# Kernel tuning notes

Hardware: AMD Instinct MI355X
Metric: run time of the kernel (lower is better)

Reference implementation:

```python
import jax, jax.numpy as jnp
import numpy as np

B, C, H, W = 4, 32, 512, 512


def _warp_add(x, flow, residual):
    # x: [B,C,H,W], flow: [B,2,H,W], residual: [B,C,H,W]
    Bs, Cs, Hs, Ws = x.shape
    # align_corners=False pixel-center base grid in [-1,1]
    gy = (jnp.arange(Hs, dtype=x.dtype) + 0.5) * (2.0 / Hs) - 1.0  # [H]
    gx = (jnp.arange(Ws, dtype=x.dtype) + 0.5) * (2.0 / Ws) - 1.0  # [W]
    grid_x = gx[None, None, :] + flow[:, 0]  # [B,H,W]
    grid_y = gy[None, :, None] + flow[:, 1]  # [B,H,W]
    # circular wrap on x only
    grid_x = jnp.mod(grid_x + 1.0, 2.0) - 1.0
    real_x = (grid_x + 1.0) * (Ws * 0.5) - 0.5
    real_y = (grid_y + 1.0) * (Hs * 0.5) - 0.5
    x0 = jnp.floor(real_x)
    y0 = jnp.floor(real_y)
    dx = real_x - x0
    dy = real_y - y0
    ix0 = x0.astype(jnp.int32)
    iy0 = y0.astype(jnp.int32)
    ix1 = ix0 + 1
    iy1 = iy0 + 1

    def valid(ix, iy):
        return (ix >= 0) & (ix < Ws) & (iy >= 0) & (iy < Hs)

    xf = x.reshape(Bs, Cs, Hs * Ws)

    def gather(ix, iy):
        v = valid(ix, iy)  # [B,H,W]
        idx = jnp.clip(iy, 0, Hs - 1) * Ws + jnp.clip(ix, 0, Ws - 1)  # [B,H,W]
        g = jnp.take_along_axis(xf, idx.reshape(Bs, 1, Hs * Ws), axis=2)  # [B,C,H*W]
        g = g.reshape(Bs, Cs, Hs, Ws)
        return jnp.where(v[:, None, :, :], g, 0.0)

    v_tl = gather(ix0, iy0)
    v_tr = gather(ix1, iy0)
    v_bl = gather(ix0, iy1)
    v_br = gather(ix1, iy1)

    w_tl = ((1.0 - dx) * (1.0 - dy))[:, None]
    w_tr = (dx * (1.0 - dy))[:, None]
    w_bl = ((1.0 - dx) * dy)[:, None]
    w_br = (dx * dy)[:, None]

    out = w_tl * v_tl + w_tr * v_tr + w_bl * v_bl + w_br * v_br + residual
    return out


def setup_inputs() -> dict:
    key = jax.random.key(0)
    k1, k2, k3 = jax.random.split(key, 3)
    x = jax.random.normal(k1, (B, C, H, W), dtype=jnp.float32)
    flow = jax.random.normal(k2, (B, 2, H, W), dtype=jnp.float32) * 0.1
    residual = jax.random.normal(k3, (B, C, H, W), dtype=jnp.float32)
    return {"x": x, "flow": flow, "residual": residual}


def reference(x, flow, residual):
    return _warp_add(x, flow, residual)
```

## Files before the change

kernel.cpp:

```cpp
#include <hip/hip_runtime.h>

#define Bdim 4
#define Cdim 32
#define Hdim 512
#define Wdim 512
#define HWdim (Hdim * Wdim)

typedef __attribute__((ext_vector_type(4))) float    f32x4;
typedef __attribute__((ext_vector_type(2))) _Float16 f16x2;
typedef __attribute__((ext_vector_type(4))) _Float16 f16x4;
typedef __attribute__((ext_vector_type(8))) _Float16 f16x8;

__global__ __launch_bounds__(256) void transpose_nhwc_half_kernel(
    const float* __restrict__ x, _Float16* __restrict__ ws)
{
    __shared__ float lds[Cdim * 132];

    const int idx = blockIdx.x;
    const int tw  = idx & 3;
    const int h   = (idx >> 2) & (Hdim - 1);
    const int b   = idx >> 11;
    const int w0  = tw * 128;
    const int t   = threadIdx.x;

    f32x4 r[4];
    #pragma unroll
    for (int i = 0; i < 4; ++i) {
        const int f4 = i * 256 + t;
        const int c  = f4 >> 5;
        const int w4 = f4 & 31;
        r[i] = *(const f32x4*)(x + (((size_t)b * Cdim + c) * Hdim + h) * Wdim + w0 + w4 * 4);
    }
    #pragma unroll
    for (int i = 0; i < 4; ++i) {
        const int f4 = i * 256 + t;
        *(f32x4*)(lds + (f4 >> 5) * 132 + (f4 & 31) * 4) = r[i];
    }
    __syncthreads();

    const size_t base = (((size_t)b * Hdim + h) * Wdim + w0) * Cdim;
    const int w_ = t >> 1;
    const int c0 = (t & 1) * 16;
    f16x8 v0, v1;
    #pragma unroll
    for (int k = 0; k < 8; ++k) v0[k] = (_Float16)lds[(c0 + k) * 132 + w_];
    #pragma unroll
    for (int k = 0; k < 8; ++k) v1[k] = (_Float16)lds[(c0 + 8 + k) * 132 + w_];
    *(f16x8*)(ws + base + (size_t)w_ * Cdim + c0)     = v0;
    *(f16x8*)(ws + base + (size_t)w_ * Cdim + c0 + 8) = v1;
}

__global__ __launch_bounds__(256) void gather_nhwc_half_kernel(
    const _Float16* __restrict__ ws,
    const float* __restrict__ flow,
    const float* __restrict__ residual,
    float* __restrict__ out)
{
    __shared__ _Float16 s_buf[4 * 64 * 34];

    const int orig = blockIdx.x;
    const int idx  = (orig & 7) * 512 + (orig >> 3);

    const int b    = idx >> 10;
    const int h    = (idx >> 1) & (Hdim - 1);
    const int w0   = (idx & 1) << 8;
    const int t    = threadIdx.x;
    const int lane = t & 63;
    const int wv   = t >> 6;

    int   off0, off1, off2, off3;
    float wt0,  wt1,  wt2,  wt3;
    {
        const int w = w0 + t;
        const int pixg = h * Wdim + w;
        const float fx = flow[((size_t)b * 2 + 0) * HWdim + pixg];
        const float fy = flow[((size_t)b * 2 + 1) * HWdim + pixg];

        float gx = ((float)w + 0.5f) * (2.0f / (float)Wdim) - 1.0f + fx;
        float gy = ((float)h + 0.5f) * (2.0f / (float)Hdim) - 1.0f + fy;

        float tm = fmodf(gx + 1.0f, 2.0f);
        if (tm < 0.0f) tm += 2.0f;
        gx = tm - 1.0f;

        const float real_x = (gx + 1.0f) * ((float)Wdim * 0.5f) - 0.5f;
        const float real_y = (gy + 1.0f) * ((float)Hdim * 0.5f) - 0.5f;

        const float x0f = floorf(real_x);
        const float y0f = floorf(real_y);
        const float dx = real_x - x0f;
        const float dy = real_y - y0f;

        const int ix0 = (int)x0f;
        const int iy0 = (int)y0f;
        const int ix1 = ix0 + 1;
        const int iy1 = iy0 + 1;

        const bool vx0 = (ix0 >= 0) && (ix0 < Wdim);
        const bool vx1 = (ix1 >= 0) && (ix1 < Wdim);
        const bool vy0 = (iy0 >= 0) && (iy0 < Hdim);
        const bool vy1 = (iy1 >= 0) && (iy1 < Hdim);

        const int cx0 = min(max(ix0, 0), Wdim - 1);
        const int cx1 = min(max(ix1, 0), Wdim - 1);
        const int cy0 = min(max(iy0, 0), Hdim - 1);
        const int cy1 = min(max(iy1, 0), Hdim - 1);

        float w_tl = (1.0f - dx) * (1.0f - dy);
        float w_tr = dx * (1.0f - dy);
        float w_bl = (1.0f - dx) * dy;
        float w_br = dx * dy;
        if (!(vx0 && vy0)) w_tl = 0.0f;
        if (!(vx1 && vy0)) w_tr = 0.0f;
        if (!(vx0 && vy1)) w_bl = 0.0f;
        if (!(vx1 && vy1)) w_br = 0.0f;

        off0 = (cy0 * Wdim + cx0) * Cdim;
        off1 = (cy0 * Wdim + cx1) * Cdim;
        off2 = (cy1 * Wdim + cx0) * Cdim;
        off3 = (cy1 * Wdim + cx1) * Cdim;
        wt0 = w_tl; wt1 = w_tr; wt2 = w_bl; wt3 = w_br;
    }

    {
        const int ci = lane & 7;
        const int c0 = ci * 4;
        const int ps = lane >> 3;
        const _Float16* xb = ws + (size_t)b * (size_t)HWdim * Cdim + c0;
        _Float16* sb = s_buf + wv * (64 * 34);

        int   co[4]; float cw[4]; f16x4 cv[4];
        {
            const int sj = ps;
            co[0] = __shfl(off0, sj, 64); co[1] = __shfl(off1, sj, 64);
            co[2] = __shfl(off2, sj, 64); co[3] = __shfl(off3, sj, 64);
            cw[0] = __shfl(wt0, sj, 64);  cw[1] = __shfl(wt1, sj, 64);
            cw[2] = __shfl(wt2, sj, 64);  cw[3] = __shfl(wt3, sj, 64);
            #pragma unroll
            for (int k = 0; k < 4; ++k) cv[k] = *(const f16x4*)(xb + co[k]);
        }

        #pragma unroll
        for (int j = 0; j < 8; ++j) {
            int   no[4]; float nw[4]; f16x4 nv[4];
            if (j < 7) {
                const int sj = (j + 1) * 8 + ps;
                no[0] = __shfl(off0, sj, 64); no[1] = __shfl(off1, sj, 64);
                no[2] = __shfl(off2, sj, 64); no[3] = __shfl(off3, sj, 64);
                nw[0] = __shfl(wt0, sj, 64);  nw[1] = __shfl(wt1, sj, 64);
                nw[2] = __shfl(wt2, sj, 64);  nw[3] = __shfl(wt3, sj, 64);
                #pragma unroll
                for (int k = 0; k < 4; ++k) nv[k] = *(const f16x4*)(xb + no[k]);
            }

            const int lpix = j * 8 + ps;
            const float a0 = cw[0] * (float)cv[0][0] + cw[1] * (float)cv[1][0]
                           + cw[2] * (float)cv[2][0] + cw[3] * (float)cv[3][0];
            const float a1 = cw[0] * (float)cv[0][1] + cw[1] * (float)cv[1][1]
                           + cw[2] * (float)cv[2][1] + cw[3] * (float)cv[3][1];
            const float a2 = cw[0] * (float)cv[0][2] + cw[1] * (float)cv[1][2]
                           + cw[2] * (float)cv[2][2] + cw[3] * (float)cv[3][2];
            const float a3 = cw[0] * (float)cv[0][3] + cw[1] * (float)cv[1][3]
                           + cw[2] * (float)cv[2][3] + cw[3] * (float)cv[3][3];

            f16x2 h01; h01[0] = (_Float16)a0; h01[1] = (_Float16)a1;
            f16x2 h23; h23[0] = (_Float16)a2; h23[1] = (_Float16)a3;
            *(f16x2*)(sb + lpix * 34 + c0)     = h01;
            *(f16x2*)(sb + lpix * 34 + c0 + 2) = h23;

            if (j < 7) {
                #pragma unroll
                for (int k = 0; k < 4; ++k) { co[k] = no[k]; cw[k] = nw[k]; cv[k] = nv[k]; }
            }
        }
    }

    __builtin_amdgcn_wave_barrier();
    asm volatile("s_waitcnt lgkmcnt(0)" ::: "memory");
    __builtin_amdgcn_sched_barrier(0);

    {
        const size_t pbase = (size_t)h * Wdim + w0 + t;
        const _Float16* row = s_buf + wv * (64 * 34) + lane * 34;
        #pragma unroll 8
        for (int cc = 0; cc < Cdim; cc += 2) {
            const f16x2 v = *(const f16x2*)(row + cc);
            const size_t gi0 = ((size_t)b * Cdim + cc) * HWdim + pbase;
            const float r0 = __builtin_nontemporal_load(residual + gi0);
            const float r1 = __builtin_nontemporal_load(residual + gi0 + HWdim);
            __builtin_nontemporal_store((float)v[0] + r0, out + gi0);
            __builtin_nontemporal_store((float)v[1] + r1, out + gi0 + HWdim);
        }
    }
}

__global__ __launch_bounds__(256) void warp_add_kernel(
    const float* __restrict__ x,
    const float* __restrict__ flow,
    const float* __restrict__ residual,
    float* __restrict__ out)
{
    int tid = blockIdx.x * blockDim.x + threadIdx.x;
    int w = tid & (Wdim - 1);
    int h = (tid >> 9) & (Hdim - 1);
    int b = tid >> 18;

    const float fx = flow[((size_t)b * 2 + 0) * HWdim + h * Wdim + w];
    const float fy = flow[((size_t)b * 2 + 1) * HWdim + h * Wdim + w];

    float gx = ((float)w + 0.5f) * (2.0f / (float)Wdim) - 1.0f + fx;
    float gy = ((float)h + 0.5f) * (2.0f / (float)Hdim) - 1.0f + fy;
    {
        float t2 = fmodf(gx + 1.0f, 2.0f);
        if (t2 < 0.0f) t2 += 2.0f;
        gx = t2 - 1.0f;
    }
    const float real_x = (gx + 1.0f) * ((float)Wdim * 0.5f) - 0.5f;
    const float real_y = (gy + 1.0f) * ((float)Hdim * 0.5f) - 0.5f;
    const float x0f = floorf(real_x);
    const float y0f = floorf(real_y);
    const float dx = real_x - x0f;
    const float dy = real_y - y0f;
    const int ix0 = (int)x0f, iy0 = (int)y0f;
    const int ix1 = ix0 + 1,  iy1 = iy0 + 1;
    const bool vx0 = (ix0 >= 0) && (ix0 < Wdim);
    const bool vx1 = (ix1 >= 0) && (ix1 < Wdim);
    const bool vy0 = (iy0 >= 0) && (iy0 < Hdim);
    const bool vy1 = (iy1 >= 0) && (iy1 < Hdim);
    const int cx0 = min(max(ix0, 0), Wdim - 1);
    const int cx1 = min(max(ix1, 0), Wdim - 1);
    const int cy0 = min(max(iy0, 0), Hdim - 1);
    const int cy1 = min(max(iy1, 0), Hdim - 1);
    float w_tl = (1.0f - dx) * (1.0f - dy);
    float w_tr = dx * (1.0f - dy);
    float w_bl = (1.0f - dx) * dy;
    float w_br = dx * dy;
    if (!(vx0 && vy0)) w_tl = 0.0f;
    if (!(vx1 && vy0)) w_tr = 0.0f;
    if (!(vx0 && vy1)) w_bl = 0.0f;
    if (!(vx1 && vy1)) w_br = 0.0f;
    const int off_tl = cy0 * Wdim + cx0;
    const int off_tr = cy0 * Wdim + cx1;
    const int off_bl = cy1 * Wdim + cx0;
    const int off_br = cy1 * Wdim + cx1;
    const size_t base = (size_t)b * Cdim * HWdim;
    const int    pix  = h * Wdim + w;
    const float* xb = x + base;
    const float* rbp = residual + base + pix;
    float*       ob = out + base + pix;
    #pragma unroll 8
    for (int c = 0; c < Cdim; ++c) {
        const float* xc = xb + (size_t)c * HWdim;
        float v = w_tl * xc[off_tl] + w_tr * xc[off_tr]
                + w_bl * xc[off_bl] + w_br * xc[off_br]
                + rbp[(size_t)c * HWdim];
        ob[(size_t)c * HWdim] = v;
    }
}

extern "C" void kernel_launch(void* const* d_in, const int* in_sizes, int n_in,
                              void* d_out, int out_size, void* d_ws, size_t ws_size,
                              hipStream_t stream) {
    const float* x        = (const float*)d_in[0];
    const float* flow     = (const float*)d_in[1];
    const float* residual = (const float*)d_in[2];
    float* out            = (float*)d_out;

    const size_t ws_needed = (size_t)Bdim * Cdim * HWdim * sizeof(_Float16);

    if (ws_size >= ws_needed) {
        _Float16* ws = (_Float16*)d_ws;
        transpose_nhwc_half_kernel<<<Bdim * Hdim * (Wdim / 128), 256, 0, stream>>>(x, ws);
        gather_nhwc_half_kernel<<<Bdim * Hdim * Wdim / 256, 256, 0, stream>>>(ws, flow, residual, out);
    } else {
        const int total = Bdim * Hdim * Wdim;
        warp_add_kernel<<<total / 256, 256, 0, stream>>>(x, flow, residual, out);
    }
}
```

Before: 344.1 us.

## Gather full channel vector per thread, drop LDS staging and shuffles

The gather kernel now has each thread handle one output pixel end to end. It loads all 32 fp16 channels of each of the four corners with 16-byte vector loads, accumulates in fp32 registers, and writes straight to the NCHW output. This removes the cross-lane shuffles, the LDS staging buffer and the wave barrier, and also skips the fp16 rounding of the interpolated value. The kernel gets launch bounds with a minimum of 6 blocks per CU, and the transpose kernel gets a swizzled block order. The cost is higher register pressure from the 32 accumulators and per-thread loads that are less coalesced.

After: 397.3 us. +15.5%, slower.

```diff
diff --git a/kernel.cpp b/kernel.cpp
--- a/kernel.cpp
+++ b/kernel.cpp
@@ -16,7 +16,9 @@
 {
     __shared__ float lds[Cdim * 132];
 
-    const int idx = blockIdx.x;
+    const int orig = blockIdx.x;
+    const int idx  = (orig & 7) * 1024 + (orig >> 3);
+
     const int tw  = idx & 3;
     const int h   = (idx >> 2) & (Hdim - 1);
     const int b   = idx >> 11;
@@ -50,14 +52,12 @@
     *(f16x8*)(ws + base + (size_t)w_ * Cdim + c0 + 8) = v1;
 }
 
-__global__ __launch_bounds__(256) void gather_nhwc_half_kernel(
+__global__ __launch_bounds__(256, 6) void gather_nhwc_half_kernel(
     const _Float16* __restrict__ ws,
     const float* __restrict__ flow,
     const float* __restrict__ residual,
     float* __restrict__ out)
 {
-    __shared__ _Float16 s_buf[4 * 64 * 34];
-
     const int orig = blockIdx.x;
     const int idx  = (orig & 7) * 512 + (orig >> 3);
 
@@ -65,11 +65,9 @@
     const int h    = (idx >> 1) & (Hdim - 1);
     const int w0   = (idx & 1) << 8;
     const int t    = threadIdx.x;
-    const int lane = t & 63;
-    const int wv   = t >> 6;
-
-    int   off0, off1, off2, off3;
-    float wt0,  wt1,  wt2,  wt3;
+
+    int   offs[4];
+    float wts[4];
     {
         const int w = w0 + t;
         const int pixg = h * Wdim + w;
@@ -115,81 +113,39 @@
         if (!(vx0 && vy1)) w_bl = 0.0f;
         if (!(vx1 && vy1)) w_br = 0.0f;
 
-        off0 = (cy0 * Wdim + cx0) * Cdim;
-        off1 = (cy0 * Wdim + cx1) * Cdim;
-        off2 = (cy1 * Wdim + cx0) * Cdim;
-        off3 = (cy1 * Wdim + cx1) * Cdim;
-        wt0 = w_tl; wt1 = w_tr; wt2 = w_bl; wt3 = w_br;
-    }
-
-    {
-        const int ci = lane & 7;
-        const int c0 = ci * 4;
-        const int ps = lane >> 3;
-        const _Float16* xb = ws + (size_t)b * (size_t)HWdim * Cdim + c0;
-        _Float16* sb = s_buf + wv * (64 * 34);
-
-        int   co[4]; float cw[4]; f16x4 cv[4];
-        {
-            const int sj = ps;
-            co[0] = __shfl(off0, sj, 64); co[1] = __shfl(off1, sj, 64);
-            co[2] = __shfl(off2, sj, 64); co[3] = __shfl(off3, sj, 64);
-            cw[0] = __shfl(wt0, sj, 64);  cw[1] = __shfl(wt1, sj, 64);
-            cw[2] = __shfl(wt2, sj, 64);  cw[3] = __shfl(wt3, sj, 64);
+        offs[0] = (cy0 * Wdim + cx0) * Cdim;
+        offs[1] = (cy0 * Wdim + cx1) * Cdim;
+        offs[2] = (cy1 * Wdim + cx0) * Cdim;
+        offs[3] = (cy1 * Wdim + cx1) * Cdim;
+        wts[0] = w_tl; wts[1] = w_tr; wts[2] = w_bl; wts[3] = w_br;
+    }
+
+    const _Float16* xb = ws + (size_t)b * (size_t)HWdim * Cdim;
+
+    float acc[Cdim];
+    #pragma unroll
+    for (int k = 0; k < Cdim; ++k) acc[k] = 0.0f;
+
+    #pragma unroll
+    for (int c = 0; c < 4; ++c) {
+        const _Float16* cp = xb + offs[c];
+        const float wc = wts[c];
+        #pragma unroll
+        for (int g = 0; g < 4; ++g) {
+            const f16x8 u = *(const f16x8*)(cp + g * 8);
             #pragma unroll
-            for (int k = 0; k < 4; ++k) cv[k] = *(const f16x4*)(xb + co[k]);
+            for (int e = 0; e < 8; ++e)
+                acc[g * 8 + e] += wc * (float)u[e];
         }
-
-        #pragma unroll
-        for (int j = 0; j < 8; ++j) {
-            int   no[4]; float nw[4]; f16x4 nv[4];
-            if (j < 7) {
-                const int sj = (j + 1) * 8 + ps;
-                no[0] = __shfl(off0, sj, 64); no[1] = __shfl(off1, sj, 64);
-                no[2] = __shfl(off2, sj, 64); no[3] = __shfl(off3, sj, 64);
-                nw[0] = __shfl(wt0, sj, 64);  nw[1] = __shfl(wt1, sj, 64);
-                nw[2] = __shfl(wt2, sj, 64);  nw[3] = __shfl(wt3, sj, 64);
-                #pragma unroll
-                for (int k = 0; k < 4; ++k) nv[k] = *(const f16x4*)(xb + no[k]);
-            }
-
-            const int lpix = j * 8 + ps;
-            const float a0 = cw[0] * (float)cv[0][0] + cw[1] * (float)cv[1][0]
-                           + cw[2] * (float)cv[2][0] + cw[3] * (float)cv[3][0];
-            const float a1 = cw[0] * (float)cv[0][1] + cw[1] * (float)cv[1][1]
-                           + cw[2] * (float)cv[2][1] + cw[3] * (float)cv[3][1];
-            const float a2 = cw[0] * (float)cv[0][2] + cw[1] * (float)cv[1][2]
-                           + cw[2] * (float)cv[2][2] + cw[3] * (float)cv[3][2];
-            const float a3 = cw[0] * (float)cv[0][3] + cw[1] * (float)cv[1][3]
-                           + cw[2] * (float)cv[2][3] + cw[3] * (float)cv[3][3];
-
-            f16x2 h01; h01[0] = (_Float16)a0; h01[1] = (_Float16)a1;
-            f16x2 h23; h23[0] = (_Float16)a2; h23[1] = (_Float16)a3;
-            *(f16x2*)(sb + lpix * 34 + c0)     = h01;
-            *(f16x2*)(sb + lpix * 34 + c0 + 2) = h23;
-
-            if (j < 7) {
-                #pragma unroll
-                for (int k = 0; k < 4; ++k) { co[k] = no[k]; cw[k] = nw[k]; cv[k] = nv[k]; }
-            }
-        }
-    }
-
-    __builtin_amdgcn_wave_barrier();
-    asm volatile("s_waitcnt lgkmcnt(0)" ::: "memory");
-    __builtin_amdgcn_sched_barrier(0);
+    }
 
     {
         const size_t pbase = (size_t)h * Wdim + w0 + t;
-        const _Float16* row = s_buf + wv * (64 * 34) + lane * 34;
-        #pragma unroll 8
-        for (int cc = 0; cc < Cdim; cc += 2) {
-            const f16x2 v = *(const f16x2*)(row + cc);
-            const size_t gi0 = ((size_t)b * Cdim + cc) * HWdim + pbase;
-            const float r0 = __builtin_nontemporal_load(residual + gi0);
-            const float r1 = __builtin_nontemporal_load(residual + gi0 + HWdim);
-            __builtin_nontemporal_store((float)v[0] + r0, out + gi0);
-            __builtin_nontemporal_store((float)v[1] + r1, out + gi0 + HWdim);
+        #pragma unroll
+        for (int cc = 0; cc < Cdim; ++cc) {
+            const size_t gi = ((size_t)b * Cdim + cc) * HWdim + pbase;
+            const float r = __builtin_nontemporal_load(residual + gi);
+            __builtin_nontemporal_store(acc[cc] + r, out + gi);
         }
     }
 }
```
